# Kernel tuning notes

Measured on AMD Instinct MI355X. Metric: run time of the kernel, lower is better.

## Reference

```python
import jax, jax.numpy as jnp
import numpy as np

SIGMA = 5.0            # isotropic, voxel_size = 1 -> sigma_voxel == sigma
TRUNCATE = 3.0         # scipy gaussian_filter default truncate used in source
LABELS = (1, 2, 3, 4, 5, 6, 7, 8)
SHAPE = (128, 128, 128)
# upper-triangle entries of the 3x3 second-moment matrix, in the source's
# sorted order: diagonal (00,11,22) first, then off-diagonals (01,12,02)
XS = np.array([0, 1, 2, 0, 1, 0])
YS = np.array([0, 1, 2, 1, 2, 2])


def _gauss_kernel(sigma):
    r = int(TRUNCATE * sigma + 0.5)
    x = np.arange(-r, r + 1, dtype=np.float32)
    k = np.exp(-0.5 * (x / sigma) ** 2)
    k /= k.sum()
    return jnp.asarray(k, dtype=jnp.float32), r


def _blur_axis(arr, kernel, r, axis):
    # separable 1D convolution along `axis` with zero ('constant', cval=0) padding
    arr = jnp.moveaxis(arr, axis, -1)
    shp = arr.shape
    x = arr.reshape(-1, 1, shp[-1])                      # (N, 1, L)
    out = jax.lax.conv_general_dilated(x, kernel.reshape(1, 1, -1), (1,), [(r, r)])
    return jnp.moveaxis(out.reshape(shp), -1, axis)


def gaussian_blur3d(arr, sigma):
    k, r = _gauss_kernel(sigma)
    for ax in (-3, -2, -1):
        arr = _blur_axis(arr, k, r, ax)
    return arr


def setup_inputs() -> dict:
    key = jax.random.key(0)
    segmentation = jax.random.randint(key, SHAPE, 0, 9, dtype=jnp.int32)
    grid = jnp.meshgrid(*(jnp.arange(s, dtype=jnp.float32) for s in SHAPE), indexing='ij')
    coords = jnp.stack(grid)                              # (3, D, H, W) world coordinates
    return {"segmentation": segmentation, "coords": coords}


def _lsd(segmentation, coords):
    xs = jnp.asarray(XS)
    ys = jnp.asarray(YS)
    acc = jnp.zeros((10,) + SHAPE, dtype=jnp.float32)
    for label in LABELS:                                  # small fixed label set
        mask = (segmentation == label).astype(jnp.float32)        # (D,H,W)
        mc = coords * mask                                        # masked coords (3,...)
        outer = mc[xs] * mc[ys]                                   # unique 2nd moments (6,...)
        stack = jnp.concatenate([mask[None], mc, outer], axis=0)  # (10, D, H, W)
        agg = gaussian_blur3d(stack, SIGMA)                       # fused: one blur for all stats
        mass = agg[0]
        denom = jnp.where(mass > 0, mass, 1.0)                    # safe; invalid voxels masked out below
        com = agg[1:4] / denom                                    # center of mass (3,...)
        # mean offset, normalized by max_distance = sigma, mapped to [0,1]
        mean_offset = ((com - coords) / SIGMA * 0.5 + 0.5) * mask
        cov = (agg[4:10] / denom - com[xs] * com[ys]) / (SIGMA * SIGMA)
        desc = jnp.concatenate([mean_offset, cov, mass[None]], axis=0)
        acc = acc + desc * mask[None]                             # descriptors[mask] += descriptor[mask]
    return jnp.clip(acc, 0.0, 1.0)


def reference(segmentation, coords):
    return _lsd(segmentation, coords)
```

## Files before the change

### kernel.cpp

```cpp
#include <hip/hip_runtime.h>
#include <hip/hip_bf16.h>
#include <hip/hip_fp16.h>
#include <math.h>


constexpr int NV = 128 * 128 * 128;
constexpr int SLICE = 128 * 128;
constexpr int R = 15;
constexpr int KL = 31;
constexpr int CSTRIDE = 160;
constexpr int RSTRIDE = 6 * CSTRIDE + 8;
constexpr int LCAP = 512;

struct Kw { float k0[KL]; float k1[KL]; float k2[KL]; };

__device__ __forceinline__ void fma4(float4& a, float w, const float4& b) {
    a.x = fmaf(w, b.x, a.x); a.y = fmaf(w, b.y, a.y);
    a.z = fmaf(w, b.z, a.z); a.w = fmaf(w, b.w, a.w);
}

__device__ __forceinline__ float4 load_mask4(const unsigned char* p, int lab) {
    unsigned int u = *(const unsigned int*)p;
    return make_float4(((u       ) & 255u) == (unsigned)lab ? 1.f : 0.f,
                       ((u >>  8 ) & 255u) == (unsigned)lab ? 1.f : 0.f,
                       ((u >> 16 ) & 255u) == (unsigned)lab ? 1.f : 0.f,
                       ((u >> 24 ) & 255u) == (unsigned)lab ? 1.f : 0.f);
}
__device__ __forceinline__ float4 load_mask4(const int* p, int lab) {
    int4 s = *(const int4*)p;
    return make_float4(s.x == lab ? 1.f : 0.f, s.y == lab ? 1.f : 0.f,
                       s.z == lab ? 1.f : 0.f, s.w == lab ? 1.f : 0.f);
}

__device__ __forceinline__ unsigned seg_pack4(const unsigned char* p) {
    return *(const unsigned int*)p;
}
__device__ __forceinline__ unsigned seg_pack4(const int* p) {
    int4 v = *(const int4*)p;
    return (unsigned)(v.x & 255) | ((unsigned)(v.y & 255) << 8) |
           ((unsigned)(v.z & 255) << 16) | ((unsigned)(v.w & 255) << 24);
}

__device__ __forceinline__ float bf_ld(const unsigned short* p) {
    return __uint_as_float(((unsigned int)(*p)) << 16);
}

__device__ __forceinline__ float4 bf4_to_f4(uint2 u) {
    return make_float4(__uint_as_float(u.x << 16),
                       __uint_as_float(u.x & 0xFFFF0000u),
                       __uint_as_float(u.y << 16),
                       __uint_as_float(u.y & 0xFFFF0000u));
}

__device__ __forceinline__ unsigned pack_bf2(float a, float b) {
    __hip_bfloat162 h = __float22bfloat162_rn(make_float2(a, b));
    return *reinterpret_cast<unsigned*>(&h);
}

template <typename ST>
__global__ __launch_bounds__(256) void pass_z_t(const ST* __restrict__ seg,
                                                unsigned short* __restrict__ A,
                                                int label0, size_t a_stride,
                                                Kw kw) {
    __shared__ float kp[3][37];
    if (threadIdx.x < 37) {
        int i = threadIdx.x, j = i - 3; bool ok = (j >= 0) && (j < KL);
        kp[0][i] = ok ? kw.k0[j] : 0.f;
        kp[1][i] = ok ? kw.k1[j] : 0.f;
        kp[2][i] = ok ? kw.k2[j] : 0.f;
    }
    __syncthreads();
    const int label = label0 + blockIdx.y;
    unsigned short* Ab = A + (size_t)blockIdx.y * a_stride;
    const int h = blockIdx.x, g = h & 7, l = h >> 3;
    const int tx = threadIdx.x & 31, ty = threadIdx.x >> 5;
    const int x0 = tx * 4;
    const int z0 = 16 * g + 4 * (l & 3);
    const int y  = (l >> 2) * 8 + ty;

    float4 acc[4][3];
#pragma unroll
    for (int t = 0; t < 4; ++t)
#pragma unroll
        for (int c = 0; c < 3; ++c) acc[t][c] = make_float4(0.f, 0.f, 0.f, 0.f);

    float4 cm = make_float4(0.f, 0.f, 0.f, 0.f), nm = cm;
    {
        int zz = z0 - R;
        if ((unsigned)zz < 128u)
            cm = load_mask4(seg + (zz * SLICE + y * 128 + x0), label);
        int zn = z0 + 1 - R;
        if ((unsigned)zn < 128u)
            nm = load_mask4(seg + (zn * SLICE + y * 128 + x0), label);
    }
    for (int j = 0; j < 34; ++j) {
        float4 fm = make_float4(0.f, 0.f, 0.f, 0.f);
        int zz = z0 + j + 2 - R;
        if (j < 32 && (unsigned)zz < 128u)
            fm = load_mask4(seg + (zz * SLICE + y * 128 + x0), label);
#pragma unroll
        for (int t = 0; t < 4; ++t) {
            int i = j - t + 3;
            fma4(acc[t][0], kp[0][i], cm);
            fma4(acc[t][1], kp[1][i], cm);
            fma4(acc[t][2], kp[2][i], cm);
        }
        cm = nm; nm = fm;
    }
#pragma unroll
    for (int t = 0; t < 4; ++t) {
        int base = (z0 + t) * SLICE + y * 128 + x0;
#pragma unroll
        for (int c = 0; c < 3; ++c) {
            float4 v = acc[t][c];
            uint2 pv = make_uint2(pack_bf2(v.x, v.y), pack_bf2(v.z, v.w));
            *reinterpret_cast<uint2*>(Ab + (size_t)c * NV + base) = pv;
        }
    }
}

__device__ __forceinline__ void conv_voxel(const unsigned short* __restrict__ Bu,
                                           int rr, int x, const Kw& kw,
                                           float o[10]) {
    const unsigned short* row = Bu + rr * RSTRIDE + (x + 1);
    float g000 = 0, g001 = 0, g002 = 0, g010 = 0, g011 = 0,
          g020 = 0, g100 = 0, g101 = 0, g110 = 0, g200 = 0;
#pragma unroll
    for (int j = 0; j < KL; ++j) {
        float w0 = kw.k0[j], w1 = kw.k1[j], w2 = kw.k2[j];
        float b0 = bf_ld(row + 0 * CSTRIDE + j);
        float b1 = bf_ld(row + 1 * CSTRIDE + j);
        float b2 = bf_ld(row + 2 * CSTRIDE + j);
        float b3 = bf_ld(row + 3 * CSTRIDE + j);
        float b4 = bf_ld(row + 4 * CSTRIDE + j);
        float b5 = bf_ld(row + 5 * CSTRIDE + j);
        g000 = fmaf(w0, b0, g000); g001 = fmaf(w1, b0, g001); g002 = fmaf(w2, b0, g002);
        g010 = fmaf(w0, b1, g010); g011 = fmaf(w1, b1, g011);
        g020 = fmaf(w0, b2, g020);
        g100 = fmaf(w0, b3, g100); g101 = fmaf(w1, b3, g101);
        g110 = fmaf(w0, b4, g110);
        g200 = fmaf(w0, b5, g200);
    }
    float mass = g000;
    float denom = (mass > 0.f) ? mass : 1.f;
    float inv = 1.f / denom;
    float p = g100 * inv, q = g010 * inv, s = g001 * inv;
    const float cs = 1.0f / 25.0f;
    o[0] = 0.5f - 0.1f * p;
    o[1] = 0.5f - 0.1f * q;
    o[2] = 0.5f - 0.1f * s;
    o[3] = (g200 * inv - p * p) * cs;
    o[4] = (g020 * inv - q * q) * cs;
    o[5] = (g002 * inv - s * s) * cs;
    o[6] = (g110 * inv - p * q) * cs;
    o[7] = (g011 * inv - q * s) * cs;
    o[8] = (g101 * inv - p * s) * cs;
    o[9] = mass;
#pragma unroll
    for (int c = 0; c < 10; ++c) o[c] = fminf(fmaxf(o[c], 0.f), 1.f);
}

__device__ __forceinline__ void do_voxel_out(const unsigned short* __restrict__ Bu,
                                             int rr, int x, int z0, int y0,
                                             float* __restrict__ out, const Kw& kw) {
    float o[10];
    conv_voxel(Bu, rr, x, kw, o);
    const int z2 = z0 + (rr >> 2), y2 = y0 + (rr & 3);
    const int v = (z2 * 128 + y2) * 128 + x;
#pragma unroll
    for (int c = 0; c < 10; ++c) out[(size_t)c * NV + v] = o[c];
}

__device__ __forceinline__ void zero_voxel(int rr, int x, int z0, int y0,
                                           float* __restrict__ out) {
    const int z2 = z0 + (rr >> 2), y2 = y0 + (rr & 3);
    const int v = (z2 * 128 + y2) * 128 + x;
#pragma unroll
    for (int c = 0; c < 10; ++c) out[(size_t)c * NV + v] = 0.f;
}

template <typename ST>
__global__ __launch_bounds__(256, 4) void pass_yx_all(
        const unsigned short* __restrict__ A,
        const ST* __restrict__ seg,
        float* __restrict__ out,
        size_t a_stride, Kw kw) {
    __shared__ float4 kq4[40];
    __shared__ __align__(16) unsigned short Bu[8 * RSTRIDE];
    __shared__ __align__(16) unsigned stage32[1024 * 5];
    __shared__ unsigned short lst[LCAP];
    __shared__ int cnt2[2];

    {
        uint4 z4 = make_uint4(0, 0, 0, 0);
        uint4* b4 = (uint4*)Bu;
        for (int i = threadIdx.x; i < 968; i += 256) b4[i] = z4;
        uint4* s4 = (uint4*)stage32;
        for (int i = threadIdx.x; i < 1280; i += 256) s4[i] = z4;
    }
    if (threadIdx.x < 40) {
        int i = threadIdx.x, j = i - 3; bool ok = (j >= 0) && (j < KL);
        kq4[i] = make_float4(ok ? kw.k0[j] : 0.f, ok ? kw.k1[j] : 0.f,
                             ok ? kw.k2[j] : 0.f, 0.f);
    }
    if (threadIdx.x == 0) { cnt2[0] = 0; cnt2[1] = 0; }

    const int b = blockIdx.x, g = b & 7, l = b >> 3;
    const int z0 = 16 * g + 2 * (l & 7);
    const int y0 = (l >> 3) * 4;

    const unsigned pk = seg_pack4(seg +
        ((z0 + (threadIdx.x >> 7)) * 128 + (y0 + ((threadIdx.x >> 5) & 3))) * 128 +
        (threadIdx.x & 31) * 4);

    const int w = threadIdx.x >> 6;
    const int zr = w & 1, cg = w >> 1;
    const int lane = threadIdx.x & 63;
    const int lx = lane & 31, lh = lane >> 5;
    const int x0 = 4 * lx;
    const int t0 = 2 * lh;
    const int zrs = (z0 + zr) * SLICE;
    const unsigned long long below_mask = (1ull << lane) - 1ull;

    __syncthreads();

    for (int labi = 0; labi < 8; ++labi) {
        const int label = 1 + labi;
        const unsigned short* Ab0 = A + (size_t)labi * a_stride;
        const unsigned short* Ab1 = Ab0 + NV;
        const unsigned short* Ab2 = Ab0 + 2 * NV;

        float4 acc[3][2];
#pragma unroll
        for (int c = 0; c < 3; ++c)
#pragma unroll
            for (int k = 0; k < 2; ++k) acc[c][k] = make_float4(0.f, 0.f, 0.f, 0.f);

        uint2 u0c = make_uint2(0u, 0u), u0n = u0c;
        uint2 u1c = u0c, u1n = u0c, u2c = u0c, u2n = u0c;
        {
            int yy = y0 - R;
            if ((unsigned)yy < 128u) {
                int base = zrs + yy * 128 + x0;
                if (cg == 0) u0c = *(const uint2*)(Ab0 + base);
                else { u1c = *(const uint2*)(Ab1 + base); u2c = *(const uint2*)(Ab2 + base); }
            }
            int yn = y0 + 1 - R;
            if ((unsigned)yn < 128u) {
                int base = zrs + yn * 128 + x0;
                if (cg == 0) u0n = *(const uint2*)(Ab0 + base);
                else { u1n = *(const uint2*)(Ab1 + base); u2n = *(const uint2*)(Ab2 + base); }
            }
        }
        for (int j = 0; j < 34; ++j) {
            uint2 f0 = make_uint2(0u, 0u), f1 = f0, f2 = f0;
            int yy = y0 + j + 2 - R;
            if (j < 32 && (unsigned)yy < 128u) {
                int base = zrs + yy * 128 + x0;
                if (cg == 0) f0 = *(const uint2*)(Ab0 + base);
                else { f1 = *(const uint2*)(Ab1 + base); f2 = *(const uint2*)(Ab2 + base); }
            }
            if (cg == 0) {
                float4 a0 = bf4_to_f4(u0c);
#pragma unroll
                for (int k = 0; k < 2; ++k) {
                    float4 wv = kq4[j + 3 - (t0 + k)];
                    fma4(acc[0][k], wv.x, a0);
                    fma4(acc[1][k], wv.y, a0);
                    fma4(acc[2][k], wv.z, a0);
                }
            } else {
                float4 a1 = bf4_to_f4(u1c), a2 = bf4_to_f4(u2c);
#pragma unroll
                for (int k = 0; k < 2; ++k) {
                    float4 wv = kq4[j + 3 - (t0 + k)];
                    fma4(acc[0][k], wv.x, a1);
                    fma4(acc[1][k], wv.y, a1);
                    fma4(acc[2][k], wv.x, a2);
                }
            }
            u0c = u0n; u1c = u1n; u2c = u2n;
            u0n = f0;  u1n = f1;  u2n = f2;
        }

        __syncthreads();

#pragma unroll
        for (int k = 0; k < 2; ++k) {
            const int row = zr * 4 + t0 + k;
#pragma unroll
            for (int c3 = 0; c3 < 3; ++c3) {
                const int c = cg * 3 + c3;
                float4 v = acc[c3][k];
                uint2 pv = make_uint2(pack_bf2(v.x, v.y), pack_bf2(v.z, v.w));
                *reinterpret_cast<uint2*>(Bu + row * RSTRIDE + c * CSTRIDE + 16 + x0) = pv;
            }
        }
        {
            int* cw = &cnt2[labi & 1];
#pragma unroll
            for (int t = 0; t < 4; ++t) {
                const int sv = (int)((pk >> (8 * t)) & 255u);
                const bool pred = (sv == label);
                unsigned long long bal = __ballot(pred);
                int base = 0;
                if (lane == 0 && bal) base = atomicAdd(cw, (int)__popcll(bal));
                base = __shfl(base, 0);
                if (pred) {
                    int pos = base + (int)__popcll(bal & below_mask);
                    if (pos < LCAP)
                        lst[pos] = (unsigned short)(4 * threadIdx.x + t);
                }
            }
            if (threadIdx.x == 0) cnt2[(labi + 1) & 1] = 0;
        }

        __syncthreads();

        const int total = cnt2[labi & 1];
        if (total <= LCAP) {
            for (int e = threadIdx.x; e < total; e += 256) {
                int ent = lst[e];
                int rr = ent >> 7, x = ent & 127;
                float o[10];
                conv_voxel(Bu, rr, x, kw, o);
                unsigned* s = stage32 + (rr * 128 + x) * 5;
#pragma unroll
                for (int i = 0; i < 5; ++i) {
                    __half2 hp = __float22half2_rn(make_float2(o[2 * i], o[2 * i + 1]));
                    s[i] = *reinterpret_cast<unsigned*>(&hp);
                }
            }
        } else {
#pragma unroll
            for (int t = 0; t < 4; ++t) {
                const int sv = (int)((pk >> (8 * t)) & 255u);
                if (sv == label) {
                    int vx = 4 * threadIdx.x + t;
                    int rr = vx >> 7, x = vx & 127;
                    float o[10];
                    conv_voxel(Bu, rr, x, kw, o);
                    unsigned* s = stage32 + vx * 5;
#pragma unroll
                    for (int i = 0; i < 5; ++i) {
                        __half2 hp = __float22half2_rn(make_float2(o[2 * i], o[2 * i + 1]));
                        s[i] = *reinterpret_cast<unsigned*>(&hp);
                    }
                }
            }
        }
    }

    __syncthreads();

    const __half* sh = (const __half*)stage32;
    for (int c = 0; c < 10; ++c) {
        float* oc = out + (size_t)c * NV;
#pragma unroll
        for (int k = 0; k < 4; ++k) {
            int idx = threadIdx.x + k * 256;
            float f = __half2float(sh[idx * 10 + c]);
            int gb = ((z0 + (idx >> 9)) * 128 + y0) * 128 + (idx & 511);
            oc[gb] = f;
        }
    }
}

template <typename ST>
__global__ __launch_bounds__(128) void pass_yx(const unsigned short* __restrict__ A,
                                               const ST* __restrict__ seg,
                                               float* __restrict__ out,
                                               int label0, size_t a_stride,
                                               Kw kw) {
    __shared__ float kp[3][37];
    __shared__ __align__(16) unsigned short Bu2[16 * RSTRIDE];
    __shared__ unsigned short lst[LCAP];
    __shared__ int cnt;

    {
        uint4 z4 = make_uint4(0, 0, 0, 0);
        uint4* b4 = (uint4*)Bu2;
        for (int i = threadIdx.x; i < 1936; i += 128) b4[i] = z4;
    }
    if (threadIdx.x < 37) {
        int i = threadIdx.x, j = i - 3; bool ok = (j >= 0) && (j < KL);
        kp[0][i] = ok ? kw.k0[j] : 0.f;
        kp[1][i] = ok ? kw.k1[j] : 0.f;
        kp[2][i] = ok ? kw.k2[j] : 0.f;
    }
    if (threadIdx.x == 0) cnt = 0;
    __syncthreads();

    const int labi = blockIdx.y;
    const int label = label0 + labi;
    const unsigned short* Ab = A + (size_t)labi * a_stride;
    const int h = blockIdx.x, g = h & 7, l = h >> 3;
    const int tx = threadIdx.x & 31, tz = threadIdx.x >> 5;
    const int x0 = tx * 4;
    const int z0 = 16 * g + 4 * (l & 3);
    const int y0 = (l >> 2) * 4;
    const int zs = (z0 + tz) * SLICE;

    const int rr_c = threadIdx.x >> 3, q0_c = threadIdx.x & 7;
    const int vrow_c = ((z0 + (rr_c >> 2)) * 128 + (y0 + (rr_c & 3))) * 128;
    unsigned pk[4];
#pragma unroll
    for (int k = 0; k < 4; ++k)
        pk[k] = seg_pack4(seg + vrow_c + 4 * (q0_c + 8 * k));

    float4 acc[6][4];
#pragma unroll
    for (int c = 0; c < 6; ++c)
#pragma unroll
        for (int t = 0; t < 4; ++t) acc[c][t] = make_float4(0.f, 0.f, 0.f, 0.f);

    uint2 c0 = make_uint2(0u, 0u), c1 = c0, c2 = c0;
    uint2 n0 = c0, n1 = c0, n2 = c0;
    {
        int yy = y0 - R;
        if ((unsigned)yy < 128u) {
            int base = zs + yy * 128 + x0;
            c0 = *(const uint2*)(Ab + base);
            c1 = *(const uint2*)(Ab + NV + base);
            c2 = *(const uint2*)(Ab + 2 * NV + base);
        }
        int yn = y0 + 1 - R;
        if ((unsigned)yn < 128u) {
            int base = zs + yn * 128 + x0;
            n0 = *(const uint2*)(Ab + base);
            n1 = *(const uint2*)(Ab + NV + base);
            n2 = *(const uint2*)(Ab + 2 * NV + base);
        }
    }
    for (int j = 0; j < 34; ++j) {
        uint2 f0 = make_uint2(0u, 0u), f1 = f0, f2 = f0;
        int yy = y0 + j + 2 - R;
        if (j < 32 && (unsigned)yy < 128u) {
            int base = zs + yy * 128 + x0;
            f0 = *(const uint2*)(Ab + base);
            f1 = *(const uint2*)(Ab + NV + base);
            f2 = *(const uint2*)(Ab + 2 * NV + base);
        }
        float4 a0 = bf4_to_f4(c0), a1 = bf4_to_f4(c1), a2 = bf4_to_f4(c2);
#pragma unroll
        for (int t = 0; t < 4; ++t) {
            int i = j - t + 3;
            float w0 = kp[0][i], w1 = kp[1][i], w2 = kp[2][i];
            fma4(acc[0][t], w0, a0);
            fma4(acc[1][t], w1, a0);
            fma4(acc[2][t], w2, a0);
            fma4(acc[3][t], w0, a1);
            fma4(acc[4][t], w1, a1);
            fma4(acc[5][t], w0, a2);
        }
        c0 = n0; c1 = n1; c2 = n2;
        n0 = f0; n1 = f1; n2 = f2;
    }
#pragma unroll
    for (int t = 0; t < 4; ++t) {
        const int row = tz * 4 + t;
#pragma unroll
        for (int c = 0; c < 6; ++c) {
            uint2 pv = make_uint2(pack_bf2(acc[c][t].x, acc[c][t].y),
                                  pack_bf2(acc[c][t].z, acc[c][t].w));
            *reinterpret_cast<uint2*>(Bu2 + row * RSTRIDE + c * CSTRIDE + 16 + x0) = pv;
        }
    }

    {
        const int lane = threadIdx.x & 63;
        const unsigned long long below_mask = (1ull << lane) - 1ull;
#pragma unroll
        for (int k = 0; k < 4; ++k) {
            const unsigned w = pk[k];
#pragma unroll
            for (int t = 0; t < 4; ++t) {
                const int sv = (int)((w >> (8 * t)) & 255u);
                const int x = 4 * (q0_c + 8 * k) + t;
                const bool mt = (sv == label);
                const bool zt = !mt && (sv < 1 || sv > 8) &&
                                (((x & 7) + 1) == label);
                const bool pred = mt | zt;
                unsigned long long bal = __ballot(pred);
                int base = 0;
                if (lane == 0 && bal) base = atomicAdd(&cnt, (int)__popcll(bal));
                base = __shfl(base, 0);
                if (pred) {
                    int pos = base + (int)__popcll(bal & below_mask);
                    if (pos < LCAP)
                        lst[pos] = (unsigned short)((rr_c << 7) | x | (zt ? 0x8000 : 0));
                }
            }
        }
    }

    __syncthreads();

    const int total = cnt;
    if (total <= LCAP) {
        for (int e = threadIdx.x; e < total; e += 128) {
            int ent = lst[e];
            int rr = (ent >> 7) & 15, x = ent & 127;
            if (ent & 0x8000) zero_voxel(rr, x, z0, y0, out);
            else do_voxel_out(Bu2, rr, x, z0, y0, out, kw);
        }
    } else {
        for (int e = threadIdx.x; e < 2048; e += 128) {
            int rr = e >> 7, x = e & 127;
            int z2 = z0 + (rr >> 2), y2 = y0 + (rr & 3);
            int sv = (int)seg[(z2 * 128 + y2) * 128 + x] & 255;
            if (sv == label)
                do_voxel_out(Bu2, rr, x, z0, y0, out, kw);
            else if ((sv < 1 || sv > 8) && (((x & 7) + 1) == label))
                zero_voxel(rr, x, z0, y0, out);
        }
    }
}

__global__ __launch_bounds__(256) void seg_to_u8(const int* __restrict__ seg,
                                                 unsigned char* __restrict__ seg8) {
    const int t = blockIdx.x * 256 + threadIdx.x;
    const int4 s = ((const int4*)seg)[t];
    ((uchar4*)seg8)[t] = make_uchar4((unsigned char)s.x, (unsigned char)s.y,
                                     (unsigned char)s.z, (unsigned char)s.w);
}

extern "C" void kernel_launch(void* const* d_in, const int* in_sizes, int n_in,
                              void* d_out, int out_size, void* d_ws, size_t ws_size,
                              hipStream_t stream) {
    const int* seg = (const int*)d_in[0];
    float* out = (float*)d_out;
    unsigned short* A = (unsigned short*)d_ws;
    const size_t AVOL = (size_t)3 * NV;

    Kw kw;
    double gg[KL], S = 0.0;
    for (int j = 0; j < KL; ++j) { double d = j - R; gg[j] = exp(-0.5 * d * d / 25.0); S += gg[j]; }
    for (int j = 0; j < KL; ++j) {
        double gn = gg[j] / S, d = j - R;
        kw.k0[j] = (float)gn;
        kw.k1[j] = (float)(-d * gn);
        kw.k2[j] = (float)(d * d * gn);
    }


    const size_t need_all = 8 * AVOL * sizeof(unsigned short) + NV;
    const size_t need_one = AVOL * sizeof(unsigned short) + NV;

    if (ws_size >= need_all) {
        unsigned char* seg8 = (unsigned char*)d_ws + 8 * AVOL * sizeof(unsigned short);
        seg_to_u8<<<dim3(2048), dim3(256), 0, stream>>>(seg, seg8);
        pass_z_t<unsigned char><<<dim3(512, 8), dim3(256), 0, stream>>>(
            seg8, A, 1, AVOL, kw);
        pass_yx_all<unsigned char><<<dim3(2048), dim3(256), 0, stream>>>(
            A, seg8, out, AVOL, kw);
    } else if (ws_size >= need_one) {
        unsigned char* seg8 = (unsigned char*)d_ws + AVOL * sizeof(unsigned short);
        seg_to_u8<<<dim3(2048), dim3(256), 0, stream>>>(seg, seg8);
        for (int label = 1; label <= 8; ++label) {
            pass_z_t<unsigned char><<<dim3(512, 1), dim3(256), 0, stream>>>(
                seg8, A, label, 0, kw);
            pass_yx<unsigned char><<<dim3(1024, 1), dim3(128), 0, stream>>>(
                A, seg8, out, label, 0, kw);
        }
    } else {
        for (int label = 1; label <= 8; ++label) {
            pass_z_t<int><<<dim3(512, 1), dim3(256), 0, stream>>>(
                seg, A, label, 0, kw);
            pass_yx<int><<<dim3(1024, 1), dim3(128), 0, stream>>>(
                A, seg, out, label, 0, kw);
        }
    }
}
```

Before: 452.1 us.

## Write descriptors directly to global, drop shared staging buffer, raise occupancy

Removes the 20 KB shared-memory fp16 staging buffer and the final per-block copy-out. Each label's matching voxels now write their fp32 results straight to global memory. Unlabeled voxels get zeros written, spread across the label iterations by x position. Segmentation bytes are kept in a small shared array so the compaction scan reads them in a lane-contiguous order, and launch bounds go from 4 to 8 blocks per CU. The intent is to cut LDS use so more blocks fit and to drop the fp16 round-trip, at the cost of scattered 4-byte global stores per voxel and channel.

```diff
diff --git a/kernel.cpp b/kernel.cpp
--- a/kernel.cpp
+++ b/kernel.cpp
@@ -1,6 +1,5 @@
 #include <hip/hip_runtime.h>
 #include <hip/hip_bf16.h>
-#include <hip/hip_fp16.h>
 #include <math.h>
 
 
@@ -180,14 +179,14 @@
 }
 
 template <typename ST>
-__global__ __launch_bounds__(256, 4) void pass_yx_all(
+__global__ __launch_bounds__(256, 8) void pass_yx_all(
         const unsigned short* __restrict__ A,
         const ST* __restrict__ seg,
         float* __restrict__ out,
         size_t a_stride, Kw kw) {
     __shared__ float4 kq4[40];
     __shared__ __align__(16) unsigned short Bu[8 * RSTRIDE];
-    __shared__ __align__(16) unsigned stage32[1024 * 5];
+    __shared__ unsigned seg_l[256];
     __shared__ unsigned short lst[LCAP];
     __shared__ int cnt2[2];
 
@@ -195,8 +194,6 @@
         uint4 z4 = make_uint4(0, 0, 0, 0);
         uint4* b4 = (uint4*)Bu;
         for (int i = threadIdx.x; i < 968; i += 256) b4[i] = z4;
-        uint4* s4 = (uint4*)stage32;
-        for (int i = threadIdx.x; i < 1280; i += 256) s4[i] = z4;
     }
     if (threadIdx.x < 40) {
         int i = threadIdx.x, j = i - 3; bool ok = (j >= 0) && (j < KL);
@@ -212,6 +209,7 @@
     const unsigned pk = seg_pack4(seg +
         ((z0 + (threadIdx.x >> 7)) * 128 + (y0 + ((threadIdx.x >> 5) & 3))) * 128 +
         (threadIdx.x & 31) * 4);
+    seg_l[threadIdx.x] = pk;
 
     const int w = threadIdx.x >> 6;
     const int zr = w & 1, cg = w >> 1;
@@ -298,10 +296,15 @@
         }
         {
             int* cw = &cnt2[labi & 1];
-#pragma unroll
-            for (int t = 0; t < 4; ++t) {
-                const int sv = (int)((pk >> (8 * t)) & 255u);
-                const bool pred = (sv == label);
+            const unsigned char* s8 = (const unsigned char*)seg_l;
+#pragma unroll
+            for (int s = 0; s < 4; ++s) {
+                const int v = (w << 8) + (s << 6) + lane;
+                const int sv = (int)s8[v];
+                const bool mt = (sv == label);
+                const bool zt = !mt && (sv < 1 || sv > 8) &&
+                                (((v & 7) + 1) == label);
+                const bool pred = mt | zt;
                 unsigned long long bal = __ballot(pred);
                 int base = 0;
                 if (lane == 0 && bal) base = atomicAdd(cw, (int)__popcll(bal));
@@ -309,7 +312,7 @@
                 if (pred) {
                     int pos = base + (int)__popcll(bal & below_mask);
                     if (pos < LCAP)
-                        lst[pos] = (unsigned short)(4 * threadIdx.x + t);
+                        lst[pos] = (unsigned short)(v | (zt ? 0x8000 : 0));
                 }
             }
             if (threadIdx.x == 0) cnt2[(labi + 1) & 1] = 0;
@@ -321,47 +324,35 @@
         if (total <= LCAP) {
             for (int e = threadIdx.x; e < total; e += 256) {
                 int ent = lst[e];
-                int rr = ent >> 7, x = ent & 127;
-                float o[10];
-                conv_voxel(Bu, rr, x, kw, o);
-                unsigned* s = stage32 + (rr * 128 + x) * 5;
-#pragma unroll
-                for (int i = 0; i < 5; ++i) {
-                    __half2 hp = __float22half2_rn(make_float2(o[2 * i], o[2 * i + 1]));
-                    s[i] = *reinterpret_cast<unsigned*>(&hp);
+                int v = ent & 1023, rr = v >> 7, x = v & 127;
+                const int gb = ((z0 + (rr >> 2)) * 128 + (y0 + (rr & 3))) * 128 + x;
+                if (ent & 0x8000) {
+#pragma unroll
+                    for (int c = 0; c < 10; ++c) out[(size_t)c * NV + gb] = 0.f;
+                } else {
+                    float o[10];
+                    conv_voxel(Bu, rr, x, kw, o);
+#pragma unroll
+                    for (int c = 0; c < 10; ++c) out[(size_t)c * NV + gb] = o[c];
                 }
             }
         } else {
 #pragma unroll
             for (int t = 0; t < 4; ++t) {
                 const int sv = (int)((pk >> (8 * t)) & 255u);
+                const int v = 4 * (int)threadIdx.x + t;
+                const int rr = v >> 7, x = v & 127;
+                const int gb = ((z0 + (rr >> 2)) * 128 + (y0 + (rr & 3))) * 128 + x;
                 if (sv == label) {
-                    int vx = 4 * threadIdx.x + t;
-                    int rr = vx >> 7, x = vx & 127;
                     float o[10];
                     conv_voxel(Bu, rr, x, kw, o);
-                    unsigned* s = stage32 + vx * 5;
-#pragma unroll
-                    for (int i = 0; i < 5; ++i) {
-                        __half2 hp = __float22half2_rn(make_float2(o[2 * i], o[2 * i + 1]));
-                        s[i] = *reinterpret_cast<unsigned*>(&hp);
-                    }
+#pragma unroll
+                    for (int c = 0; c < 10; ++c) out[(size_t)c * NV + gb] = o[c];
+                } else if ((sv < 1 || sv > 8) && (((v & 7) + 1) == label)) {
+#pragma unroll
+                    for (int c = 0; c < 10; ++c) out[(size_t)c * NV + gb] = 0.f;
                 }
             }
-        }
-    }
-
-    __syncthreads();
-
-    const __half* sh = (const __half*)stage32;
-    for (int c = 0; c < 10; ++c) {
-        float* oc = out + (size_t)c * NV;
-#pragma unroll
-        for (int k = 0; k < 4; ++k) {
-            int idx = threadIdx.x + k * 256;
-            float f = __half2float(sh[idx * 10 + c]);
-            int gb = ((z0 + (idx >> 9)) * 128 + y0) * 128 + (idx & 511);
-            oc[gb] = f;
         }
     }
 }
```

After: 643.8 us. 42.4% more time.
